# Kernel optimization log

Hardware: AMD Instinct MI355X
Metric: run time of the kernel (lower is better)

## Reference

```python
import jax, jax.numpy as jnp
import numpy as np

N_EMBED = 384
HEAD_SIZE = 64
B, T = 128, 512


def rope(x):
    # Faithful to source: fres = 1/1000**(arange(0,dim,2)//dim) -> integer
    # floor-div makes the exponent all zeros, so fres == 1 everywhere.
    Bx, Tx, D = x.shape
    half = D // 2
    fres = jnp.ones((half,), dtype=jnp.float32)
    ang = jnp.arange(Tx, dtype=jnp.float32)[:, None] * fres[None, :]  # (T, half)
    cos, sin = jnp.cos(ang), jnp.sin(ang)
    xr = x.reshape(Bx, Tx, half, 2)
    xe, xo = xr[..., 0], xr[..., 1]
    oe = xe * cos - xo * sin
    oo = xe * sin + xo * cos
    return jnp.stack([oe, oo], axis=-1).reshape(Bx, Tx, D)


def setup_inputs() -> dict:
    key = jax.random.key(0)
    ks = jax.random.split(key, 7)
    s = 1.0 / np.sqrt(N_EMBED)
    return {
        "x": jax.random.normal(ks[0], (B, T, N_EMBED), dtype=jnp.float32),
        "wq": jax.random.uniform(ks[1], (N_EMBED, HEAD_SIZE), jnp.float32, -s, s),
        "bq": jax.random.uniform(ks[2], (HEAD_SIZE,), jnp.float32, -s, s),
        "wk": jax.random.uniform(ks[3], (N_EMBED, HEAD_SIZE), jnp.float32, -s, s),
        "bk": jax.random.uniform(ks[4], (HEAD_SIZE,), jnp.float32, -s, s),
        "wv": jax.random.uniform(ks[5], (N_EMBED, HEAD_SIZE), jnp.float32, -s, s),
        "bv": jax.random.uniform(ks[6], (HEAD_SIZE,), jnp.float32, -s, s),
    }


def reference(x, wq, bq, wk, bk, wv, bv):
    Bx, Tx, C = x.shape  # C = n_embed; scale uses C per the source (not head_size)
    q = rope(x @ wq + bq)
    k = rope(x @ wk + bk)
    wei = jnp.einsum("bqd,bkd->bqk", q, k) * (C ** -0.5)  # (B, T, T)
    causal = jnp.tril(jnp.ones((Tx, Tx), dtype=bool))
    wei = jnp.where(causal, wei, -jnp.inf)
    wei = jax.nn.softmax(wei, axis=-1)
    v = x @ wv + bv
    return jnp.einsum("bqk,bkd->bqd", wei, v)
```

## Files before the change

kernel.cpp:

```cpp
#include <hip/hip_runtime.h>

#define TSEQ 512
#define NB   128
#define CDIM 384
#define HD   64
#define QSCALE 0.051031036307982884f
#define MBIAS  8.0f

typedef _Float16 half8  __attribute__((ext_vector_type(8)));
typedef _Float16 half4  __attribute__((ext_vector_type(4)));
typedef float    floatx4 __attribute__((ext_vector_type(4)));

typedef __attribute__((address_space(3))) unsigned int lds_u32;
typedef const __attribute__((address_space(1))) unsigned int g_u32;

__device__ __forceinline__ void load_lds16(const void* g, void* l) {
    __builtin_amdgcn_global_load_lds((g_u32*)g, (lds_u32*)l, 16, 0, 0);
}

__global__ void prep_w(const float* __restrict__ wq, const float* __restrict__ wk,
                       const float* __restrict__ wv, _Float16* __restrict__ Wt)
{
    int i = blockIdx.x * 256 + threadIdx.x;
    const int per = CDIM * HD;
    if (i >= 3 * per) return;
    int mat = i / per;
    int rem = i - mat * per;
    int k = rem / HD;
    int n = rem - k * HD;
    const float* w = (mat == 0) ? wq : ((mat == 1) ? wk : wv);
    Wt[((size_t)mat * HD + n) * CDIM + k] = (_Float16)w[rem];
}

__global__ __launch_bounds__(256) void qkv_gemm(
    const float* __restrict__ x, const _Float16* __restrict__ Wt,
    const float* __restrict__ bq, const float* __restrict__ bk,
    const float* __restrict__ bv,
    _Float16* __restrict__ Qw, _Float16* __restrict__ Kw,
    _Float16* __restrict__ Vtw, int b0)
{
    __shared__ __align__(16) float    xs[8 * 64 * 8];
    __shared__ __align__(16) _Float16 wsb[8 * 192 * 8];

    const int tid  = threadIdx.x;
    const int wave = tid >> 6;
    const int lane = tid & 63;
    const int l16  = lane & 15;
    const int quad = lane >> 4;

    const int row0 = blockIdx.x * 64;
    const size_t rowg = (size_t)b0 * TSEQ + row0;

    floatx4 acc[12];
#pragma unroll
    for (int i = 0; i < 12; ++i)
#pragma unroll
        for (int r = 0; r < 4; ++r) acc[i][r] = 0.f;

    for (int c = 0; c < 6; ++c) {
        const int kk0 = c * 64;

#pragma unroll
        for (int i = 0; i < 4; ++i) {
            const int I    = wave * 4 + i;
            const int cell = I * 32 + (lane >> 1);
            const int kblk = cell >> 6;
            const int m    = cell & 63;
            const int kin0 = (lane & 1) * 4;
            const float* src = x + (rowg + m) * CDIM + kk0 + kblk * 8 + kin0;
            load_lds16(src, (char*)xs + I * 1024);
        }
#pragma unroll
        for (int i = 0; i < 6; ++i) {
            const int I2   = wave * 6 + i;
            const int c2   = I2 * 64 + lane;
            const int kblk = c2 / 192;
            const int n    = c2 - kblk * 192;
            const _Float16* src = Wt + (size_t)n * CDIM + kk0 + kblk * 8;
            load_lds16(src, (char*)wsb + I2 * 1024);
        }
        __syncthreads();

#pragma unroll
        for (int kb2 = 0; kb2 < 2; ++kb2) {
            const int kblk = kb2 * 4 + quad;
            const float* ap = xs + ((size_t)kblk * 64 + wave * 16 + l16) * 8;
            floatx4 a0 = *(const floatx4*)ap;
            floatx4 a1 = *(const floatx4*)(ap + 4);
            half8 a;
#pragma unroll
            for (int jj = 0; jj < 8; ++jj)
                a[jj] = (_Float16)(jj < 4 ? a0[jj] : a1[jj - 4]);
            const _Float16* bp = wsb + ((size_t)kblk * 192 + l16) * 8;
#pragma unroll
            for (int i = 0; i < 12; ++i) {
                half8 bb = *(const half8*)(bp + i * 128);
                acc[i] = __builtin_amdgcn_mfma_f32_16x16x32_f16(a, bb, acc[i], 0, 0, 0);
            }
        }
        __syncthreads();
    }

    float bq4[4], bk4[4], bv4[4];
#pragma unroll
    for (int s4 = 0; s4 < 4; ++s4) {
        const int cc = s4 * 16 + l16;
        bq4[s4] = bq[cc]; bk4[s4] = bk[cc]; bv4[s4] = bv[cc];
    }
    const int t00  = (row0 & (TSEQ - 1)) + wave * 16 + quad * 4;
    const int bidx = row0 >> 9;
    const int rowb = row0 + wave * 16 + quad * 4;

#pragma unroll
    for (int r = 0; r < 4; ++r) {
        const int t = t00 + r;
        const float st = sinf((float)t);
        const float ct = cosf((float)t);
        const int row = rowb + r;
#pragma unroll
        for (int s4 = 0; s4 < 4; ++s4) {
            const int cc = s4 * 16 + l16;
            float vq = acc[s4][r] + bq4[s4];
            float pq = __shfl_xor(vq, 1);
            vq = (cc & 1) ? (pq * st + vq * ct) : (vq * ct - pq * st);
            Qw[(size_t)row * HD + cc] = (_Float16)(vq * QSCALE);
            float vk = acc[4 + s4][r] + bk4[s4];
            float pk = __shfl_xor(vk, 1);
            vk = (cc & 1) ? (pk * st + vk * ct) : (vk * ct - pk * st);
            Kw[(size_t)row * HD + cc] = (_Float16)vk;
        }
    }
#pragma unroll
    for (int s4 = 0; s4 < 4; ++s4) {
        const int cc = s4 * 16 + l16;
        half4 vpack;
#pragma unroll
        for (int r = 0; r < 4; ++r) vpack[r] = (_Float16)(acc[8 + s4][r] + bv4[s4]);
        *(half4*)(Vtw + ((size_t)bidx * HD + cc) * TSEQ + t00) = vpack;
    }
}

__global__ __launch_bounds__(256) void attn_kernel(
    const _Float16* __restrict__ Qw, const _Float16* __restrict__ Kw,
    const _Float16* __restrict__ Vtw, float* __restrict__ out, int b0)
{
    const int qt   = blockIdx.x;
    const int bl   = blockIdx.y;
    const int tid  = threadIdx.x;
    const int wave = tid >> 6;
    const int lane = tid & 63;
    const int l16  = lane & 15;
    const int quad = lane >> 4;

    __shared__ __align__(16) _Float16 pbuf[4][16][72];

    const _Float16* Qb = Qw  + (size_t)bl * TSEQ * HD;
    const _Float16* Kb = Kw  + (size_t)bl * TSEQ * HD;
    const _Float16* Vb = Vtw + (size_t)bl * HD * TSEQ;

    const int qA = qt * 128 + wave * 16;
    const int qB = qA + 64;
    const int jd = 2 * qt;

    half8 aQA0 = *(const half8*)(Qb + (size_t)(qA + l16) * HD + quad * 8);
    half8 aQA1 = *(const half8*)(Qb + (size_t)(qA + l16) * HD + 32 + quad * 8);
    half8 aQB0 = *(const half8*)(Qb + (size_t)(qB + l16) * HD + quad * 8);
    half8 aQB1 = *(const half8*)(Qb + (size_t)(qB + l16) * HD + 32 + quad * 8);

    half8 ones;
#pragma unroll
    for (int jj = 0; jj < 8; ++jj) ones[jj] = (_Float16)1.f;

    floatx4 accO[8], accL[2];
#pragma unroll
    for (int i = 0; i < 8; ++i)
#pragma unroll
        for (int r = 0; r < 4; ++r) accO[i][r] = 0.f;
#pragma unroll
    for (int s = 0; s < 2; ++s)
#pragma unroll
        for (int r = 0; r < 4; ++r) accL[s][r] = 0.f;

    for (int j = 0; j <= jd + 1; ++j) {
        const int kb = j * 64;

        half8 bK0[4], bK1[4], bV0[4], bV1[4];
#pragma unroll
        for (int s4 = 0; s4 < 4; ++s4) {
            const _Float16* kp = Kb + (size_t)(kb + s4 * 16 + l16) * HD + quad * 8;
            bK0[s4] = *(const half8*)(kp);
            bK1[s4] = *(const half8*)(kp + 32);
            const _Float16* vp = Vb + (size_t)(s4 * 16 + l16) * TSEQ + kb + quad * 8;
            bV0[s4] = *(const half8*)(vp);
            bV1[s4] = *(const half8*)(vp + 32);
        }

        if (j <= jd) {
            floatx4 st4[4];
#pragma unroll
            for (int s4 = 0; s4 < 4; ++s4) {
#pragma unroll
                for (int r = 0; r < 4; ++r) st4[s4][r] = 0.f;
                st4[s4] = __builtin_amdgcn_mfma_f32_16x16x32_f16(bK0[s4], aQA0, st4[s4], 0, 0, 0);
                st4[s4] = __builtin_amdgcn_mfma_f32_16x16x32_f16(bK1[s4], aQA1, st4[s4], 0, 0, 0);
            }
            const int qrow = qA + l16;
#pragma unroll
            for (int s4 = 0; s4 < 4; ++s4) {
                half4 w;
#pragma unroll
                for (int r = 0; r < 4; ++r) {
                    float p = __expf(fminf(st4[s4][r], 18.f) - MBIAS);
                    if (j == jd) {
                        const int kcol = kb + s4 * 16 + quad * 4 + r;
                        if (kcol > qrow) p = 0.f;
                    }
                    w[r] = (_Float16)p;
                }
                *(half4*)(&pbuf[wave][l16][s4 * 16 + quad * 4]) = w;
            }
            half8 aP0 = *(const half8*)(&pbuf[wave][l16][quad * 8]);
            half8 aP1 = *(const half8*)(&pbuf[wave][l16][32 + quad * 8]);
#pragma unroll
            for (int s4 = 0; s4 < 4; ++s4) {
                accO[s4] = __builtin_amdgcn_mfma_f32_16x16x32_f16(aP0, bV0[s4], accO[s4], 0, 0, 0);
                accO[s4] = __builtin_amdgcn_mfma_f32_16x16x32_f16(aP1, bV1[s4], accO[s4], 0, 0, 0);
            }
            accL[0] = __builtin_amdgcn_mfma_f32_16x16x32_f16(aP0, ones, accL[0], 0, 0, 0);
            accL[0] = __builtin_amdgcn_mfma_f32_16x16x32_f16(aP1, ones, accL[0], 0, 0, 0);
        }

        {
            floatx4 st4[4];
#pragma unroll
            for (int s4 = 0; s4 < 4; ++s4) {
#pragma unroll
                for (int r = 0; r < 4; ++r) st4[s4][r] = 0.f;
                st4[s4] = __builtin_amdgcn_mfma_f32_16x16x32_f16(bK0[s4], aQB0, st4[s4], 0, 0, 0);
                st4[s4] = __builtin_amdgcn_mfma_f32_16x16x32_f16(bK1[s4], aQB1, st4[s4], 0, 0, 0);
            }
            const int qrow = qB + l16;
#pragma unroll
            for (int s4 = 0; s4 < 4; ++s4) {
                half4 w;
#pragma unroll
                for (int r = 0; r < 4; ++r) {
                    float p = __expf(fminf(st4[s4][r], 18.f) - MBIAS);
                    if (j == jd + 1) {
                        const int kcol = kb + s4 * 16 + quad * 4 + r;
                        if (kcol > qrow) p = 0.f;
                    }
                    w[r] = (_Float16)p;
                }
                *(half4*)(&pbuf[wave][l16][s4 * 16 + quad * 4]) = w;
            }
            half8 aP0 = *(const half8*)(&pbuf[wave][l16][quad * 8]);
            half8 aP1 = *(const half8*)(&pbuf[wave][l16][32 + quad * 8]);
#pragma unroll
            for (int s4 = 0; s4 < 4; ++s4) {
                accO[4 + s4] = __builtin_amdgcn_mfma_f32_16x16x32_f16(aP0, bV0[s4], accO[4 + s4], 0, 0, 0);
                accO[4 + s4] = __builtin_amdgcn_mfma_f32_16x16x32_f16(aP1, bV1[s4], accO[4 + s4], 0, 0, 0);
            }
            accL[1] = __builtin_amdgcn_mfma_f32_16x16x32_f16(aP0, ones, accL[1], 0, 0, 0);
            accL[1] = __builtin_amdgcn_mfma_f32_16x16x32_f16(aP1, ones, accL[1], 0, 0, 0);
        }
    }

#pragma unroll
    for (int s = 0; s < 2; ++s) {
        const int qbase = (s == 0) ? qA : qB;
        float inv[4];
#pragma unroll
        for (int r = 0; r < 4; ++r) inv[r] = 1.f / accL[s][r];
#pragma unroll
        for (int s4 = 0; s4 < 4; ++s4) {
            const int dcol = s4 * 16 + l16;
#pragma unroll
            for (int r = 0; r < 4; ++r) {
                const int qr = qbase + quad * 4 + r;
                out[((size_t)(b0 + bl) * TSEQ + qr) * HD + dcol] =
                    accO[s * 4 + s4][r] * inv[r];
            }
        }
    }
}

extern "C" void kernel_launch(void* const* d_in, const int* in_sizes, int n_in,
                              void* d_out, int out_size, void* d_ws, size_t ws_size,
                              hipStream_t stream)
{
    char* ws = (char*)d_ws;
    _Float16* Wt = (_Float16*)ws;
    char* qkv_base = ws + 147456;

    const size_t per_b = (size_t)3 * TSEQ * HD * sizeof(_Float16);
    size_t avail = (ws_size > (size_t)147456) ? ws_size - 147456 : per_b;
    int nbc = (int)(avail / per_b);
    if (nbc > NB) nbc = NB;
    if (nbc < 1)  nbc = 1;

    const size_t chunk_elems = (size_t)nbc * TSEQ * HD;
    _Float16* Qw  = (_Float16*)qkv_base;
    _Float16* Kw  = Qw + chunk_elems;
    _Float16* Vtw = Kw + chunk_elems;

    prep_w<<<dim3((3 * CDIM * HD + 255) / 256), dim3(256), 0, stream>>>(
        (const float*)d_in[1], (const float*)d_in[3], (const float*)d_in[5], Wt);

    for (int b0 = 0; b0 < NB; b0 += nbc) {
        const int nb = (NB - b0 < nbc) ? (NB - b0) : nbc;
        qkv_gemm<<<dim3(nb * 8), dim3(256), 0, stream>>>(
            (const float*)d_in[0], Wt, (const float*)d_in[2], (const float*)d_in[4],
            (const float*)d_in[6], Qw, Kw, Vtw, b0);
        attn_kernel<<<dim3(4, nb), dim3(256), 0, stream>>>(
            Qw, Kw, Vtw, (float*)d_out, b0);
    }
}
```

Before: 212.8 us.

## Double-buffer QKV GEMM with swizzled LDS and split attention KV across wave pairs

The QKV GEMM now prepacks the weights into per-chunk tiles, uses 32-wide K chunks with a double-buffered LDS pipeline, and XOR-swizzles the x tile to avoid bank conflicts. The attention kernel doubles its grid, pairs each query tile with its mirrored tile for causal balance, and splits the KV loop between two waves whose partial accumulators are merged through LDS. It also remaps blocks so that a batch stays on one XCD and raises wave priority around MFMA sections. These changes target load latency in the GEMM and under-occupancy and load imbalance in attention, at the cost of extra LDS and a reduction step.

```diff
diff --git a/kernel.cpp b/kernel.cpp
--- a/kernel.cpp
+++ b/kernel.cpp
@@ -19,28 +19,28 @@
 }
 
 __global__ void prep_w(const float* __restrict__ wq, const float* __restrict__ wk,
-                       const float* __restrict__ wv, _Float16* __restrict__ Wt)
+                       const float* __restrict__ wv, _Float16* __restrict__ Wp)
 {
     int i = blockIdx.x * 256 + threadIdx.x;
-    const int per = CDIM * HD;
-    if (i >= 3 * per) return;
-    int mat = i / per;
-    int rem = i - mat * per;
-    int k = rem / HD;
-    int n = rem - k * HD;
+    if (i >= 3 * CDIM * HD) return;
+    int c    = i / 6144;  int r  = i - c * 6144;
+    int kblk = r / 1536;  int r2 = r - kblk * 1536;
+    int n    = r2 >> 3;   int kin = r2 & 7;
+    int k    = c * 32 + kblk * 8 + kin;
+    int mat  = n / 64;    int col = n - mat * 64;
     const float* w = (mat == 0) ? wq : ((mat == 1) ? wk : wv);
-    Wt[((size_t)mat * HD + n) * CDIM + k] = (_Float16)w[rem];
+    Wp[i] = (_Float16)w[k * HD + col];
 }
 
 __global__ __launch_bounds__(256) void qkv_gemm(
-    const float* __restrict__ x, const _Float16* __restrict__ Wt,
+    const float* __restrict__ x, const _Float16* __restrict__ Wp,
     const float* __restrict__ bq, const float* __restrict__ bk,
     const float* __restrict__ bv,
     _Float16* __restrict__ Qw, _Float16* __restrict__ Kw,
     _Float16* __restrict__ Vtw, int b0)
 {
-    __shared__ __align__(16) float    xs[8 * 64 * 8];
-    __shared__ __align__(16) _Float16 wsb[8 * 192 * 8];
+    __shared__ __align__(16) float    xs[2][64 * 32];
+    __shared__ __align__(16) _Float16 wsb[2][6144];
 
     const int tid  = threadIdx.x;
     const int wave = tid >> 6;
@@ -51,55 +51,62 @@
     const int row0 = blockIdx.x * 64;
     const size_t rowg = (size_t)b0 * TSEQ + row0;
 
+    const int xr = lane >> 3;
+    const int xu = lane & 7;
+    size_t xoff[2];
+#pragma unroll
+    for (int i = 0; i < 2; ++i) {
+        const int m = (wave * 2 + i) * 8 + xr;
+        xoff[i] = (rowg + m) * CDIM + (size_t)((xu ^ xr) << 2);
+    }
+    int woff[3];
+#pragma unroll
+    for (int i = 0; i < 3; ++i) woff[i] = (wave * 3 + i) * 512 + lane * 8;
+
     floatx4 acc[12];
 #pragma unroll
     for (int i = 0; i < 12; ++i)
 #pragma unroll
         for (int r = 0; r < 4; ++r) acc[i][r] = 0.f;
 
-    for (int c = 0; c < 6; ++c) {
-        const int kk0 = c * 64;
-
-#pragma unroll
-        for (int i = 0; i < 4; ++i) {
-            const int I    = wave * 4 + i;
-            const int cell = I * 32 + (lane >> 1);
-            const int kblk = cell >> 6;
-            const int m    = cell & 63;
-            const int kin0 = (lane & 1) * 4;
-            const float* src = x + (rowg + m) * CDIM + kk0 + kblk * 8 + kin0;
-            load_lds16(src, (char*)xs + I * 1024);
-        }
-#pragma unroll
-        for (int i = 0; i < 6; ++i) {
-            const int I2   = wave * 6 + i;
-            const int c2   = I2 * 64 + lane;
-            const int kblk = c2 / 192;
-            const int n    = c2 - kblk * 192;
-            const _Float16* src = Wt + (size_t)n * CDIM + kk0 + kblk * 8;
-            load_lds16(src, (char*)wsb + I2 * 1024);
+#define STAGE(cc, bi) do {                                                    \
+    _Pragma("unroll")                                                         \
+    for (int i_ = 0; i_ < 2; ++i_)                                            \
+        load_lds16(x + xoff[i_] + (cc) * 32,                                  \
+                   (char*)&xs[bi][0] + (wave * 2 + i_) * 1024);               \
+    _Pragma("unroll")                                                         \
+    for (int i_ = 0; i_ < 3; ++i_)                                            \
+        load_lds16(Wp + (cc) * 6144 + woff[i_],                               \
+                   (char*)&wsb[bi][0] + (wave * 3 + i_) * 1024);              \
+} while (0)
+
+    STAGE(0, 0);
+    __syncthreads();
+
+#pragma unroll
+    for (int c = 0; c < 12; ++c) {
+        if (c < 11) STAGE(c + 1, (c + 1) & 1);
+
+        const float*    xb = xs[c & 1];
+        const _Float16* wb = wsb[c & 1];
+        const int m  = wave * 16 + l16;
+        const int mh = l16 & 7;
+        const int j0 = quad * 2;
+        floatx4 a0 = *(const floatx4*)(xb + m * 32 + ((j0 ^ mh) << 2));
+        floatx4 a1 = *(const floatx4*)(xb + m * 32 + (((j0 + 1) ^ mh) << 2));
+        half8 a;
+#pragma unroll
+        for (int jj = 0; jj < 8; ++jj)
+            a[jj] = (_Float16)(jj < 4 ? a0[jj] : a1[jj - 4]);
+        const _Float16* bp = wb + ((size_t)quad * 192 + l16) * 8;
+#pragma unroll
+        for (int i = 0; i < 12; ++i) {
+            half8 bb = *(const half8*)(bp + i * 128);
+            acc[i] = __builtin_amdgcn_mfma_f32_16x16x32_f16(a, bb, acc[i], 0, 0, 0);
         }
         __syncthreads();
-
-#pragma unroll
-        for (int kb2 = 0; kb2 < 2; ++kb2) {
-            const int kblk = kb2 * 4 + quad;
-            const float* ap = xs + ((size_t)kblk * 64 + wave * 16 + l16) * 8;
-            floatx4 a0 = *(const floatx4*)ap;
-            floatx4 a1 = *(const floatx4*)(ap + 4);
-            half8 a;
-#pragma unroll
-            for (int jj = 0; jj < 8; ++jj)
-                a[jj] = (_Float16)(jj < 4 ? a0[jj] : a1[jj - 4]);
-            const _Float16* bp = wsb + ((size_t)kblk * 192 + l16) * 8;
-#pragma unroll
-            for (int i = 0; i < 12; ++i) {
-                half8 bb = *(const half8*)(bp + i * 128);
-                acc[i] = __builtin_amdgcn_mfma_f32_16x16x32_f16(a, bb, acc[i], 0, 0, 0);
-            }
-        }
-        __syncthreads();
-    }
+    }
+#undef STAGE
 
     float bq4[4], bk4[4], bv4[4];
 #pragma unroll
@@ -144,23 +151,36 @@
     const _Float16* __restrict__ Qw, const _Float16* __restrict__ Kw,
     const _Float16* __restrict__ Vtw, float* __restrict__ out, int b0)
 {
-    const int qt   = blockIdx.x;
-    const int bl   = blockIdx.y;
+    int bx, bl;
+    {
+        const int lin = blockIdx.y * 8 + blockIdx.x;
+        if ((gridDim.y & 7) == 0) {
+            const int per = gridDim.y >> 3;
+            const int xcd = lin & 7;
+            const int k2  = lin >> 3;
+            bl = xcd * per + (k2 >> 3);
+            bx = k2 & 7;
+        } else { bx = blockIdx.x; bl = blockIdx.y; }
+    }
     const int tid  = threadIdx.x;
     const int wave = tid >> 6;
     const int lane = tid & 63;
     const int l16  = lane & 15;
     const int quad = lane >> 4;
 
+    const int pr  = bx * 2 + (wave & 1);
+    const int h   = wave >> 1;
+    const int qA  = pr * 16;
+    const int qB  = (31 - pr) * 16;
+    const int jdA = pr >> 2;
+    const int jdB = (31 - pr) >> 2;
+
     __shared__ __align__(16) _Float16 pbuf[4][16][72];
+    __shared__ __align__(16) floatx4  mbuf[2][10][64];
 
     const _Float16* Qb = Qw  + (size_t)bl * TSEQ * HD;
     const _Float16* Kb = Kw  + (size_t)bl * TSEQ * HD;
     const _Float16* Vb = Vtw + (size_t)bl * HD * TSEQ;
-
-    const int qA = qt * 128 + wave * 16;
-    const int qB = qA + 64;
-    const int jd = 2 * qt;
 
     half8 aQA0 = *(const half8*)(Qb + (size_t)(qA + l16) * HD + quad * 8);
     half8 aQA1 = *(const half8*)(Qb + (size_t)(qA + l16) * HD + 32 + quad * 8);
@@ -181,7 +201,7 @@
 #pragma unroll
         for (int r = 0; r < 4; ++r) accL[s][r] = 0.f;
 
-    for (int j = 0; j <= jd + 1; ++j) {
+    for (int j = h; j <= jdB; j += 2) {
         const int kb = j * 64;
 
         half8 bK0[4], bK1[4], bV0[4], bV1[4];
@@ -195,8 +215,9 @@
             bV1[s4] = *(const half8*)(vp + 32);
         }
 
-        if (j <= jd) {
+        if (j <= jdA) {
             floatx4 st4[4];
+            __builtin_amdgcn_s_setprio(1);
 #pragma unroll
             for (int s4 = 0; s4 < 4; ++s4) {
 #pragma unroll
@@ -204,6 +225,7 @@
                 st4[s4] = __builtin_amdgcn_mfma_f32_16x16x32_f16(bK0[s4], aQA0, st4[s4], 0, 0, 0);
                 st4[s4] = __builtin_amdgcn_mfma_f32_16x16x32_f16(bK1[s4], aQA1, st4[s4], 0, 0, 0);
             }
+            __builtin_amdgcn_s_setprio(0);
             const int qrow = qA + l16;
 #pragma unroll
             for (int s4 = 0; s4 < 4; ++s4) {
@@ -211,7 +233,7 @@
 #pragma unroll
                 for (int r = 0; r < 4; ++r) {
                     float p = __expf(fminf(st4[s4][r], 18.f) - MBIAS);
-                    if (j == jd) {
+                    if (j == jdA) {
                         const int kcol = kb + s4 * 16 + quad * 4 + r;
                         if (kcol > qrow) p = 0.f;
                     }
@@ -221,6 +243,7 @@
             }
             half8 aP0 = *(const half8*)(&pbuf[wave][l16][quad * 8]);
             half8 aP1 = *(const half8*)(&pbuf[wave][l16][32 + quad * 8]);
+            __builtin_amdgcn_s_setprio(1);
 #pragma unroll
             for (int s4 = 0; s4 < 4; ++s4) {
                 accO[s4] = __builtin_amdgcn_mfma_f32_16x16x32_f16(aP0, bV0[s4], accO[s4], 0, 0, 0);
@@ -228,10 +251,12 @@
             }
             accL[0] = __builtin_amdgcn_mfma_f32_16x16x32_f16(aP0, ones, accL[0], 0, 0, 0);
             accL[0] = __builtin_amdgcn_mfma_f32_16x16x32_f16(aP1, ones, accL[0], 0, 0, 0);
+            __builtin_amdgcn_s_setprio(0);
         }
 
         {
             floatx4 st4[4];
+            __builtin_amdgcn_s_setprio(1);
 #pragma unroll
             for (int s4 = 0; s4 < 4; ++s4) {
 #pragma unroll
@@ -239,6 +264,7 @@
                 st4[s4] = __builtin_amdgcn_mfma_f32_16x16x32_f16(bK0[s4], aQB0, st4[s4], 0, 0, 0);
                 st4[s4] = __builtin_amdgcn_mfma_f32_16x16x32_f16(bK1[s4], aQB1, st4[s4], 0, 0, 0);
             }
+            __builtin_amdgcn_s_setprio(0);
             const int qrow = qB + l16;
 #pragma unroll
             for (int s4 = 0; s4 < 4; ++s4) {
@@ -246,7 +272,7 @@
 #pragma unroll
                 for (int r = 0; r < 4; ++r) {
                     float p = __expf(fminf(st4[s4][r], 18.f) - MBIAS);
-                    if (j == jd + 1) {
+                    if (j == jdB) {
                         const int kcol = kb + s4 * 16 + quad * 4 + r;
                         if (kcol > qrow) p = 0.f;
                     }
@@ -256,6 +282,7 @@
             }
             half8 aP0 = *(const half8*)(&pbuf[wave][l16][quad * 8]);
             half8 aP1 = *(const half8*)(&pbuf[wave][l16][32 + quad * 8]);
+            __builtin_amdgcn_s_setprio(1);
 #pragma unroll
             for (int s4 = 0; s4 < 4; ++s4) {
                 accO[4 + s4] = __builtin_amdgcn_mfma_f32_16x16x32_f16(aP0, bV0[s4], accO[4 + s4], 0, 0, 0);
@@ -263,7 +290,31 @@
             }
             accL[1] = __builtin_amdgcn_mfma_f32_16x16x32_f16(aP0, ones, accL[1], 0, 0, 0);
             accL[1] = __builtin_amdgcn_mfma_f32_16x16x32_f16(aP1, ones, accL[1], 0, 0, 0);
-        }
+            __builtin_amdgcn_s_setprio(0);
+        }
+    }
+
+    const int slot = wave & 1;
+    if (h == 1) {
+#pragma unroll
+        for (int i = 0; i < 8; ++i) mbuf[slot][i][lane] = accO[i];
+        mbuf[slot][8][lane] = accL[0];
+        mbuf[slot][9][lane] = accL[1];
+    }
+    __syncthreads();
+    if (h == 1) return;
+
+#pragma unroll
+    for (int i = 0; i < 8; ++i) {
+        floatx4 t = mbuf[slot][i][lane];
+#pragma unroll
+        for (int r = 0; r < 4; ++r) accO[i][r] += t[r];
+    }
+    {
+        floatx4 t8 = mbuf[slot][8][lane];
+        floatx4 t9 = mbuf[slot][9][lane];
+#pragma unroll
+        for (int r = 0; r < 4; ++r) { accL[0][r] += t8[r]; accL[1][r] += t9[r]; }
     }
 
 #pragma unroll
@@ -290,7 +341,7 @@
                               hipStream_t stream)
 {
     char* ws = (char*)d_ws;
-    _Float16* Wt = (_Float16*)ws;
+    _Float16* Wp = (_Float16*)ws;
     char* qkv_base = ws + 147456;
 
     const size_t per_b = (size_t)3 * TSEQ * HD * sizeof(_Float16);
@@ -305,14 +356,14 @@
     _Float16* Vtw = Kw + chunk_elems;
 
     prep_w<<<dim3((3 * CDIM * HD + 255) / 256), dim3(256), 0, stream>>>(
-        (const float*)d_in[1], (const float*)d_in[3], (const float*)d_in[5], Wt);
+        (const float*)d_in[1], (const float*)d_in[3], (const float*)d_in[5], Wp);
 
     for (int b0 = 0; b0 < NB; b0 += nbc) {
         const int nb = (NB - b0 < nbc) ? (NB - b0) : nbc;
         qkv_gemm<<<dim3(nb * 8), dim3(256), 0, stream>>>(
-            (const float*)d_in[0], Wt, (const float*)d_in[2], (const float*)d_in[4],
+            (const float*)d_in[0], Wp, (const float*)d_in[2], (const float*)d_in[4],
             (const float*)d_in[6], Qw, Kw, Vtw, b0);
-        attn_kernel<<<dim3(4, nb), dim3(256), 0, stream>>>(
+        attn_kernel<<<dim3(8, nb), dim3(256), 0, stream>>>(
             Qw, Kw, Vtw, (float*)d_out, b0);
     }
 }
```

New measurement: 210.6 us. Within noise of the previous version (-1.0%).
